# Optimization experiments

Hardware: AMD Instinct MI355X
Metric: run time of the kernel (lower is better)

Reference implementation:

```python
import jax, jax.numpy as jnp
import numpy as np
from jax import lax

T = 32
TAU = 2.0
ALPHA = 2.0
V_TH = 1.0
V_RESET = 0.0
MAX_ACTION = 1.0
HID = 750

# ATan surrogate spike function (spikingjelly surrogate.ATan with alpha=2.0)
@jax.custom_vjp
def atan_spike(x):
    return (x >= 0.0).astype(x.dtype)

def _spike_fwd(x):
    return atan_spike(x), x

def _spike_bwd(x, g):
    # d/dx [1/pi * atan(pi/2 * alpha * x) + 1/2] = (alpha/2) / (1 + (pi/2*alpha*x)^2)
    return (g * (ALPHA / 2.0) / (1.0 + (jnp.pi / 2.0 * ALPHA * x) ** 2),)

atan_spike.defvjp(_spike_fwd, _spike_bwd)


def lif_seq(x_seq):
    """MultiStepLIFNode with decay_input=True, hard reset. x_seq: [T,B,D] -> spikes [T,B,D]."""
    def step(v, x):
        h = v + (x - (v - V_RESET)) / TAU  # neuronal_charge
        s = atan_spike(h - V_TH)           # neuronal_fire
        v_new = h * (1.0 - s) + V_RESET * s  # hard reset
        return v_new, s
    v0 = jnp.zeros_like(x_seq[0])
    _, spikes = lax.scan(step, v0, x_seq)
    return spikes


def seq_linear(x_seq, W, b):
    # x_seq: [T,B,I], W: [O,I], b: [O]
    return jnp.einsum('tbi,oi->tbo', x_seq, W) + b


def nonspiking_out(x_seq):
    # NonSpikingLIFNode.forward receives the whole [T,B,D] seq (override bypasses the step loop):
    # v starts at 0 scalar -> v = 0 + (x - (0 - v_reset))/tau = x/tau (v_reset=0), shape [T,B,D]
    return (x_seq + V_RESET) / TAU - 0.0 + 0.0 if False else x_seq / TAU


def setup_inputs() -> dict:
    key = jax.random.key(0)
    ks = jax.random.split(key, 20)
    B, SD, AD, LD = 2048, 256, 64, 128
    def lin(kw, kb, o, i):
        bound = 1.0 / np.sqrt(i)
        W = jax.random.uniform(kw, (o, i), jnp.float32, -bound, bound)
        b = jax.random.uniform(kb, (o,), jnp.float32, -bound, bound)
        return W, b
    W1, b1 = lin(ks[0], ks[1], HID, SD + AD)
    W2, b2 = lin(ks[2], ks[3], HID, HID)
    Wm, bm = lin(ks[4], ks[5], LD, HID)
    Wls, bls = lin(ks[6], ks[7], LD, HID)
    Wd1, bd1 = lin(ks[8], ks[9], HID, SD + LD)
    Wd2, bd2 = lin(ks[10], ks[11], HID, HID)
    Wd3, bd3 = lin(ks[12], ks[13], AD, HID)
    return {
        'state': jax.random.normal(ks[14], (B, SD), jnp.float32),
        'action': jax.random.normal(ks[15], (B, AD), jnp.float32),
        'eps': jax.random.normal(ks[16], (B, LD), jnp.float32),
        'W1': W1, 'b1': b1, 'W2': W2, 'b2': b2,
        'Wm': Wm, 'bm': bm, 'Wls': Wls, 'bls': bls,
        'Wd1': Wd1, 'bd1': bd1, 'Wd2': Wd2, 'bd2': bd2, 'Wd3': Wd3, 'bd3': bd3,
    }


def reference(state, action, eps, W1, b1, W2, b2, Wm, bm, Wls, bls, Wd1, bd1, Wd2, bd2, Wd3, bd3):
    B = state.shape[0]
    # Encoder
    x = jnp.concatenate([state, action], axis=1)            # [B, SD+AD]
    x_seq = jnp.broadcast_to(x, (T,) + x.shape)             # repeat(T,1,1)
    z = lif_seq(seq_linear(x_seq, W1, b1))                  # e1
    z = lif_seq(seq_linear(z, W2, b2))                      # e2
    mean = jnp.max(seq_linear(z, Wm, bm) / TAU, axis=0)     # NonSpiking v = x/tau, then max over T
    log_std = jnp.max(seq_linear(z, Wls, bls) / TAU, axis=0)
    log_std = jnp.clip(log_std, -4.0, 15.0)
    std = jnp.exp(log_std)
    zlat = mean + std * eps
    # Decoder
    d_in = jnp.concatenate([state, zlat], axis=1)
    d_seq = jnp.broadcast_to(d_in, (T,) + d_in.shape)
    a = lif_seq(seq_linear(d_seq, Wd1, bd1))
    a = lif_seq(seq_linear(a, Wd2, bd2))
    a = jnp.max(seq_linear(a, Wd3, bd3) / TAU, axis=0)
    u = MAX_ACTION * jnp.tanh(a)
    return (u, mean, std)
```

## Files before the change

kernel.cpp:

```cpp
#include <hip/hip_runtime.h>
#include <math.h>

#define TT   32
#define NB   2048
#define SDIM 256
#define ADIM 64
#define LDIM 128
#define HID  750
#define KP   768
#define KW   24
#define EIN  320
#define DIN  384
#define NSTEP 12

typedef float    f32x4 __attribute__((ext_vector_type(4)));
typedef int      i32x4 __attribute__((ext_vector_type(4)));
typedef unsigned u32x4 __attribute__((ext_vector_type(4)));

__device__ __forceinline__ f32x4 mfma16(u32x4 a, u32x4 b, f32x4 c) {
    asm("v_mfma_f32_16x16x32_bf16 %0, %1, %2, %0" : "+v"(c) : "v"(a), "v"(b));
    return c;
}
__device__ __forceinline__ i32x4 mfma_i8(u32x4 a, u32x4 b, i32x4 c) {
    asm("v_mfma_i32_16x16x64_i8 %0, %1, %2, %0" : "+v"(c) : "v"(a), "v"(b));
    return c;
}

__device__ __forceinline__ void gload_lds16(void* lds, const void* g) {
    __builtin_amdgcn_global_load_lds(
        (const __attribute__((address_space(1))) unsigned int*)g,
        (__attribute__((address_space(3))) unsigned int*)lds, 16, 0, 0);
}

__device__ __forceinline__ void bfsplit(float v, unsigned& hb, unsigned& lb) {
    unsigned u = __float_as_uint(v);
    hb = (u + 0x7FFFu + ((u >> 16) & 1u)) >> 16;
    float res = v - __uint_as_float(hb << 16);
    unsigned u2 = __float_as_uint(res);
    lb = (u2 + 0x7FFFu + ((u2 >> 16) & 1u)) >> 16;
}

#define I8_E1 589824
#define I8_E2 1179648
#define I8_E3 1277952
#define I8_E4 1376256
#define I8_E5 1425408
__global__ void wsplit_i8_all(const float* __restrict__ W2,
                              const float* __restrict__ Wd2,
                              const float* __restrict__ Wm,
                              const float* __restrict__ Wls,
                              const float* __restrict__ Wd3,
                              char* __restrict__ W2h,  char* __restrict__ W2l,
                              char* __restrict__ Wd2h, char* __restrict__ Wd2l,
                              char* __restrict__ WmlsH, char* __restrict__ WmlsL,
                              char* __restrict__ Wu3h, char* __restrict__ Wu3l) {
    int i = blockIdx.x * blockDim.x + threadIdx.x;
    if (i >= I8_E5) return;
    const float* src; char* dh; char* dl; int rvalid, o_base;
    if (i < I8_E1)      { src = W2;  dh = W2h;  dl = W2l;  rvalid = HID;  o_base = 0; }
    else if (i < I8_E2) { i -= I8_E1; src = Wd2; dh = Wd2h; dl = Wd2l; rvalid = HID;  o_base = 0; }
    else if (i < I8_E3) { i -= I8_E2; src = Wm;  dh = WmlsH; dl = WmlsL; rvalid = LDIM; o_base = 0; }
    else if (i < I8_E4) { i -= I8_E3; src = Wls; dh = WmlsH; dl = WmlsL; rvalid = LDIM; o_base = 128; }
    else                { i -= I8_E4; src = Wd3; dh = Wu3h; dl = Wu3l; rvalid = ADIM; o_base = 0; }
    int r = i / KP, k = i % KP;
    float v = (r < rvalid && k < HID) ? src[r * HID + k] : 0.f;
    int q = (int)rintf(v * 524288.f);
    int lo = (q << 24) >> 24;
    int hi = (q - lo) >> 8;
    int o = o_base + r;
    size_t di = (size_t)((o >> 6) * NSTEP + (k >> 6)) * 4096
              + ((k >> 4) & 3) * 1024 + (o & 63) * 16 + (k & 15);
    dh[di] = (char)hi;
    dl[di] = (char)lo;
}

#define BF_E1 245760
#define BF_E2 540672
__global__ void wsplit_bf_all(const float* __restrict__ W1,
                              const float* __restrict__ Wd1,
                              unsigned short* __restrict__ W1h,
                              unsigned short* __restrict__ W1l,
                              unsigned short* __restrict__ Wd1h,
                              unsigned short* __restrict__ Wd1l) {
    int i = blockIdx.x * blockDim.x + threadIdx.x;
    if (i >= BF_E2) return;
    const float* src; unsigned short* dh; unsigned short* dl; int K, KS;
    if (i < BF_E1) { src = W1; dh = W1h; dl = W1l; K = EIN; KS = 5; }
    else { i -= BF_E1; src = Wd1; dh = Wd1h; dl = Wd1l; K = DIN; KS = 6; }
    int r = i / K, k = i % K;
    float v = (r < HID) ? src[r * K + k] : 0.f;
    unsigned hb, lb;
    bfsplit(v, hb, lb);
    size_t di = ((size_t)((r >> 6) * KS + (k >> 6)) * 8
               + ((k >> 5) & 1) * 4 + ((k >> 3) & 3)) * 512 + (r & 63) * 8 + (k & 7);
    dh[di] = (unsigned short)hb;
    dl[di] = (unsigned short)lb;
}

__global__ void concat_xsplit_enc(const float* __restrict__ state,
                                  const float* __restrict__ action,
                                  unsigned short* __restrict__ Xh,
                                  unsigned short* __restrict__ Xl) {
    int t = blockIdx.x * blockDim.x + threadIdx.x;
    if (t >= NB * (EIN / 8)) return;
    int b = t & (NB - 1), c8 = t >> 11;
    float vals[8];
    if (c8 < SDIM / 8) {
        const float* src = state + (size_t)b * SDIM + c8 * 8;
#pragma unroll
        for (int j = 0; j < 8; ++j) vals[j] = src[j];
    } else {
        const float* src = action + (size_t)b * ADIM + (c8 * 8 - SDIM);
#pragma unroll
        for (int j = 0; j < 8; ++j) vals[j] = src[j];
    }
    unsigned hs[8], ls[8];
#pragma unroll
    for (int j = 0; j < 8; ++j) bfsplit(vals[j], hs[j], ls[j]);
    u32x4 ph, pl;
#pragma unroll
    for (int j = 0; j < 4; ++j) {
        ph[j] = hs[2 * j] | (hs[2 * j + 1] << 16);
        pl[j] = ls[2 * j] | (ls[2 * j + 1] << 16);
    }
    *(u32x4*)(Xh + (size_t)t * 8) = ph;
    *(u32x4*)(Xl + (size_t)t * 8) = pl;
}

__global__ void latent_xsplit(const float* __restrict__ mean_ws,
                              const float* __restrict__ ls_ws,
                              const float* __restrict__ eps,
                              const float* __restrict__ state,
                              float* __restrict__ out,
                              unsigned short* __restrict__ Xh,
                              unsigned short* __restrict__ Xl) {
    int t = blockIdx.x * blockDim.x + threadIdx.x;
    if (t >= NB * (DIN / 8)) return;
    int b = t & (NB - 1), c8 = t >> 11;
    float vals[8];
    if (c8 < SDIM / 8) {
        const float* src = state + (size_t)b * SDIM + c8 * 8;
#pragma unroll
        for (int j = 0; j < 8; ++j) vals[j] = src[j];
    } else {
        int o0 = c8 * 8 - SDIM;
#pragma unroll
        for (int j = 0; j < 8; ++j) {
            int o = o0 + j;
            float m = mean_ws[(size_t)b * LDIM + o];
            float l = ls_ws[(size_t)b * LDIM + o];
            l = fminf(fmaxf(l, -4.0f), 15.0f);
            float s = expf(l);
            vals[j] = m + s * eps[(size_t)b * LDIM + o];
            out[NB * ADIM + (size_t)b * LDIM + o] = m;
            out[NB * ADIM + NB * LDIM + (size_t)b * LDIM + o] = s;
        }
    }
    unsigned hs[8], ls[8];
#pragma unroll
    for (int j = 0; j < 8; ++j) bfsplit(vals[j], hs[j], ls[j]);
    u32x4 ph, pl;
#pragma unroll
    for (int j = 0; j < 4; ++j) {
        ph[j] = hs[2 * j] | (hs[2 * j + 1] << 16);
        pl[j] = ls[2 * j] | (ls[2 * j + 1] << 16);
    }
    *(u32x4*)(Xh + (size_t)t * 8) = ph;
    *(u32x4*)(Xl + (size_t)t * 8) = pl;
}

template<int KS>
__global__ __launch_bounds__(256)
void lif1(const unsigned short* __restrict__ Ah,
          const unsigned short* __restrict__ Al,
          const unsigned short* __restrict__ Wh,
          const unsigned short* __restrict__ Wl,
          const float* __restrict__ bias,
          unsigned* __restrict__ obitsT) {
    __shared__ __align__(16) char smraw[32768];
    const int tid = threadIdx.x, wave = tid >> 6, l = tid & 63;
    const int kg = l >> 4, li = l & 15;
    const int nb = blockIdx.x, n0 = nb * 64, mb = blockIdx.y;
    const int r0 = mb * 128 + wave * 32;
    f32x4 acc[2][4] = {};

    auto stage = [&](int buf, int step) {
        const char* sH = (const char*)(Wh + (size_t)(nb * KS + step) * 4096);
        const char* sL = (const char*)(Wl + (size_t)(nb * KS + step) * 4096);
        char* d = smraw + buf * 16384;
#pragma unroll
        for (int j = 0; j < 2; ++j) {
            gload_lds16(d + j * 4096 + tid * 16, sH + j * 4096 + tid * 16);
            gload_lds16(d + 8192 + j * 4096 + tid * 16, sL + j * 4096 + tid * 16);
        }
    };

    stage(0, 0);
    for (int step = 0; step < KS; ++step) {
        asm volatile("s_waitcnt vmcnt(0)" ::: "memory");
        __builtin_amdgcn_s_barrier();
        __builtin_amdgcn_sched_barrier(0);
        u32x4 ah[2][2], al2[2][2];
#pragma unroll
        for (int kc = 0; kc < 2; ++kc)
#pragma unroll
            for (int mt = 0; mt < 2; ++mt) {
                int r = r0 + mt * 16 + li;
                size_t aoff = ((size_t)(step * 8 + kc * 4 + kg) * NB + r) * 8;
                ah[kc][mt]  = *(const u32x4*)(Ah + aoff);
                al2[kc][mt] = *(const u32x4*)(Al + aoff);
            }
        if (step + 1 < KS) stage((step + 1) & 1, step + 1);
        const char* bufB = smraw + (step & 1) * 16384;
        __builtin_amdgcn_s_setprio(1);
#pragma unroll
        for (int kc = 0; kc < 2; ++kc) {
#pragma unroll
            for (int nt = 0; nt < 4; ++nt) {
                int boff = (kc * 4 + kg) * 1024 + (nt * 16 + li) * 16;
                u32x4 bh = *(const u32x4*)(bufB + boff);
                u32x4 bl = *(const u32x4*)(bufB + 8192 + boff);
#pragma unroll
                for (int mt = 0; mt < 2; ++mt) {
                    acc[mt][nt] = mfma16(ah[kc][mt], bh, acc[mt][nt]);
                    acc[mt][nt] = mfma16(ah[kc][mt], bl, acc[mt][nt]);
                    acc[mt][nt] = mfma16(al2[kc][mt], bh, acc[mt][nt]);
                }
            }
        }
        __builtin_amdgcn_s_setprio(0);
    }
    __syncthreads();

    unsigned* Sb = (unsigned*)smraw;
#pragma unroll
    for (int nt = 0; nt < 4; ++nt) {
        int o = n0 + nt * 16 + li;
        float bo = (o < HID) ? bias[o] : 0.f;
#pragma unroll
        for (int mt = 0; mt < 2; ++mt)
#pragma unroll
            for (int r = 0; r < 4; ++r) {
                float c = acc[mt][nt][r] + bo;
                float v = 0.f;
                unsigned sb = 0u;
#pragma unroll
                for (int t = 0; t < TT; ++t) {
                    float h = 0.5f * (v + c);
                    if (h >= 1.0f) { sb |= (1u << t); v = 0.f; }
                    else           { v = h; }
                }
                Sb[(wave * 32 + mt * 16 + kg * 4 + r) * 64 + nt * 16 + li] = sb;
            }
    }
    __syncthreads();

    for (int rr = 0; rr < 32; ++rr) {
        int row = wave * 32 + rr;
        unsigned wv = Sb[row * 64 + l];
        unsigned myw = 0;
#pragma unroll
        for (int t = 0; t < TT; ++t) {
            unsigned long long m = __ballot((wv >> t) & 1u);
            if ((l & 31) == t) myw = (l < 32) ? (unsigned)m : (unsigned)(m >> 32);
        }
        int b = mb * 128 + row;
        obitsT[((size_t)b * KW + nb * 2 + (l >= 32)) * TT + (l & 31)] = myw;
    }
}

template<int EPI>
__global__ __launch_bounds__(256)
void bitgemm(const unsigned* __restrict__ bitsT,
             const char* __restrict__ Wh,
             const char* __restrict__ Wl,
             const float* __restrict__ bias,
             const float* __restrict__ bias2,
             unsigned* __restrict__ obitsT,
             float* __restrict__ o0,
             float* __restrict__ o1) {
    __shared__ __align__(16) char smraw[34816];
    const int tid = threadIdx.x;
    const int wave = tid >> 6, l = tid & 63;
    const int kg = l >> 4, li = l & 15;
    const int nb = blockIdx.x, n0 = nb * 64;
    const int by = blockIdx.y;
    const int bb = by * 8 + wave * 2;

    i32x4 acc[4][4][2] = {};

    auto stage = [&](int buf, int step) {
        const char* sH = Wh + (size_t)(nb * NSTEP + step) * 4096;
        const char* sL = Wl + (size_t)(nb * NSTEP + step) * 4096;
        char* d = smraw + buf * 8192;
        gload_lds16(d + tid * 16, sH + tid * 16);
        gload_lds16(d + 4096 + tid * 16, sL + tid * 16);
    };
    auto aidx = [&](int mt, int step) -> size_t {
        int b = bb + (mt >> 1);
        int t = (mt & 1) * 16 + li;
        return ((size_t)b * KW + step * 2 + (kg >> 1)) * TT + t;
    };

    stage(0, 0);
    stage(1, 1);
    unsigned aw[4], awn[4];
#pragma unroll
    for (int mt = 0; mt < 4; ++mt) aw[mt] = bitsT[aidx(mt, 0)];

    for (int step = 0; step < NSTEP; ++step) {
        asm volatile("s_waitcnt vmcnt(6)" ::: "memory");
        __builtin_amdgcn_s_barrier();
        __builtin_amdgcn_sched_barrier(0);
        if (step + 2 < NSTEP) stage((step + 2) % 3, step + 2);
        if (step + 1 < NSTEP) {
#pragma unroll
            for (int mt = 0; mt < 4; ++mt) awn[mt] = bitsT[aidx(mt, step + 1)];
        }
        const char* bufB = smraw + (step % 3) * 8192;
        const unsigned fld = (kg & 1) * 16;
        u32x4 afrag[4];
#pragma unroll
        for (int mt = 0; mt < 4; ++mt) {
            unsigned w = aw[mt] >> fld;
            u32x4 a;
#pragma unroll
            for (int j = 0; j < 4; ++j)
                a[j] = __umul24((w >> (4 * j)) & 0xFu, 0x00204081u) & 0x01010101u;
            afrag[mt] = a;
        }
        __builtin_amdgcn_s_setprio(1);
#pragma unroll
        for (int nt = 0; nt < 4; ++nt) {
            int boff = kg * 1024 + (nt * 16 + li) * 16;
            u32x4 bh = *(const u32x4*)(bufB + boff);
            u32x4 bl = *(const u32x4*)(bufB + 4096 + boff);
#pragma unroll
            for (int mt = 0; mt < 4; ++mt) {
                acc[mt][nt][0] = mfma_i8(afrag[mt], bh, acc[mt][nt][0]);
                acc[mt][nt][1] = mfma_i8(afrag[mt], bl, acc[mt][nt][1]);
            }
        }
        __builtin_amdgcn_s_setprio(0);
#pragma unroll
        for (int mt = 0; mt < 4; ++mt) aw[mt] = awn[mt];
    }
    __syncthreads();

    float* Sf = (float*)smraw;
#pragma unroll
    for (int p = 0; p < 2; ++p) {
#pragma unroll
        for (int mt = 0; mt < 4; ++mt)
#pragma unroll
            for (int ntl = 0; ntl < 2; ++ntl) {
                int nt = p * 2 + ntl;
#pragma unroll
                for (int r = 0; r < 4; ++r) {
                    int cmb = (acc[mt][nt][0][r] << 8) + acc[mt][nt][1][r];
                    Sf[(wave * 64 + mt * 16 + kg * 4 + r) * 34 + ntl * 16 + li]
                        = (float)cmb * (1.f / 524288.f);
                }
            }
        __syncthreads();

        int lb = tid >> 5, col = tid & 31;
        int o = n0 + p * 32 + col;
        int b = by * 8 + lb;
        if (EPI == 0) {
            float bo = (o < HID) ? bias[o] : 0.f;
            float v = 0.f;
            unsigned sb = 0u;
#pragma unroll
            for (int t = 0; t < TT; ++t) {
                float h = 0.5f * (v + Sf[(lb * 32 + t) * 34 + col] + bo);
                if (h >= 1.0f) { sb |= (1u << t); v = 0.f; }
                else           { v = h; }
            }
            if (o >= HID) sb = 0u;
            unsigned myw = 0;
#pragma unroll
            for (int t = 0; t < TT; ++t) {
                unsigned long long m = __ballot((sb >> t) & 1u);
                if ((l & 31) == t) myw = (l < 32) ? (unsigned)m : (unsigned)(m >> 32);
            }
            int bw = by * 8 + wave * 2 + (l >= 32);
            obitsT[((size_t)bw * KW + nb * 2 + p) * TT + (l & 31)] = myw;
        } else {
            float mx = -1e30f;
#pragma unroll
            for (int t = 0; t < TT; ++t)
                mx = fmaxf(mx, Sf[(lb * 32 + t) * 34 + col]);
            if (EPI == 1) {
                float bo = (o < LDIM) ? bias[o] : bias2[o - LDIM];
                float val = 0.5f * (mx + bo);
                if (o < LDIM) o0[(size_t)b * LDIM + o] = val;
                else          o1[(size_t)b * LDIM + (o - LDIM)] = val;
            } else {
                o0[(size_t)b * ADIM + o] = tanhf(0.5f * (mx + bias[o]));
            }
        }
        __syncthreads();
    }
}

extern "C" void kernel_launch(void* const* d_in, const int* in_sizes, int n_in,
                              void* d_out, int out_size, void* d_ws, size_t ws_size,
                              hipStream_t stream) {
    const float* state  = (const float*)d_in[0];
    const float* action = (const float*)d_in[1];
    const float* eps    = (const float*)d_in[2];
    const float* W1  = (const float*)d_in[3];
    const float* b1  = (const float*)d_in[4];
    const float* W2  = (const float*)d_in[5];
    const float* b2  = (const float*)d_in[6];
    const float* Wm  = (const float*)d_in[7];
    const float* bm  = (const float*)d_in[8];
    const float* Wls = (const float*)d_in[9];
    const float* bls = (const float*)d_in[10];
    const float* Wd1 = (const float*)d_in[11];
    const float* bd1 = (const float*)d_in[12];
    const float* Wd2 = (const float*)d_in[13];
    const float* bd2 = (const float*)d_in[14];
    const float* Wd3 = (const float*)d_in[15];
    const float* bd3 = (const float*)d_in[16];
    float* out = (float*)d_out;

    char* ws = (char*)d_ws;
    size_t off = 0;
    auto alloc = [&](size_t bytes) {
        void* p = ws + off;
        off += (bytes + 255) & ~(size_t)255;
        return p;
    };
    unsigned*       bitsT_a = (unsigned*)alloc((size_t)NB * TT * KW * 4);
    unsigned*       bitsT_b = (unsigned*)alloc((size_t)NB * TT * KW * 4);
    float*          mean_ws = (float*)   alloc((size_t)NB * LDIM * 4);
    float*          ls_ws   = (float*)   alloc((size_t)NB * LDIM * 4);
    unsigned short* Xh      = (unsigned short*)alloc((size_t)NB * DIN * 2);
    unsigned short* Xl      = (unsigned short*)alloc((size_t)NB * DIN * 2);
    char*           W2h     = (char*)alloc((size_t)KP * KP);
    char*           W2l     = (char*)alloc((size_t)KP * KP);
    char*           Wd2h    = (char*)alloc((size_t)KP * KP);
    char*           Wd2l    = (char*)alloc((size_t)KP * KP);
    char*           WmlsH   = (char*)alloc((size_t)256 * KP);
    char*           WmlsL   = (char*)alloc((size_t)256 * KP);
    char*           Wu3h    = (char*)alloc((size_t)64 * KP);
    char*           Wu3l    = (char*)alloc((size_t)64 * KP);
    unsigned short* W1h     = (unsigned short*)alloc((size_t)KP * EIN * 2);
    unsigned short* W1l     = (unsigned short*)alloc((size_t)KP * EIN * 2);
    unsigned short* Wd1h    = (unsigned short*)alloc((size_t)KP * DIN * 2);
    unsigned short* Wd1l    = (unsigned short*)alloc((size_t)KP * DIN * 2);

    dim3 blk(256);

    wsplit_i8_all<<<(I8_E5 + 255) / 256, blk, 0, stream>>>(
        W2, Wd2, Wm, Wls, Wd3, W2h, W2l, Wd2h, Wd2l, WmlsH, WmlsL, Wu3h, Wu3l);
    wsplit_bf_all<<<(BF_E2 + 255) / 256, blk, 0, stream>>>(
        W1, Wd1, W1h, W1l, Wd1h, Wd1l);

    concat_xsplit_enc<<<(NB * (EIN / 8) + 255) / 256, blk, 0, stream>>>(state, action, Xh, Xl);
    lif1<5><<<dim3(12, 16), blk, 0, stream>>>(Xh, Xl, W1h, W1l, b1, bitsT_a);
    bitgemm<0><<<dim3(12, NB / 8), blk, 0, stream>>>(bitsT_a, W2h, W2l, b2, nullptr,
                                                     bitsT_b, nullptr, nullptr);
    bitgemm<1><<<dim3(4, NB / 8), blk, 0, stream>>>(bitsT_b, WmlsH, WmlsL, bm, bls,
                                                    nullptr, mean_ws, ls_ws);
    latent_xsplit<<<(NB * (DIN / 8) + 255) / 256, blk, 0, stream>>>(
        mean_ws, ls_ws, eps, state, out, Xh, Xl);

    lif1<6><<<dim3(12, 16), blk, 0, stream>>>(Xh, Xl, Wd1h, Wd1l, bd1, bitsT_a);
    bitgemm<0><<<dim3(12, NB / 8), blk, 0, stream>>>(bitsT_a, Wd2h, Wd2l, bd2, nullptr,
                                                     bitsT_b, nullptr, nullptr);
    bitgemm<2><<<dim3(1, NB / 8), blk, 0, stream>>>(bitsT_b, Wu3h, Wu3l, bd3, nullptr,
                                                    nullptr, out, nullptr);
}
```

Before: 263.5 us.

## Halve bitgemm batch tile to one row per wave with four-deep LDS ring

```diff
diff --git a/kernel.cpp b/kernel.cpp
--- a/kernel.cpp
+++ b/kernel.cpp
@@ -279,54 +279,39 @@
              unsigned* __restrict__ obitsT,
              float* __restrict__ o0,
              float* __restrict__ o1) {
-    __shared__ __align__(16) char smraw[34816];
+    __shared__ __align__(16) char smraw[32768];
     const int tid = threadIdx.x;
-    const int wave = tid >> 6, l = tid & 63;
+    const int w = tid >> 6, l = tid & 63;
     const int kg = l >> 4, li = l & 15;
     const int nb = blockIdx.x, n0 = nb * 64;
     const int by = blockIdx.y;
-    const int bb = by * 8 + wave * 2;
-
-    i32x4 acc[4][4][2] = {};
-
-    auto stage = [&](int buf, int step) {
-        const char* sH = Wh + (size_t)(nb * NSTEP + step) * 4096;
-        const char* sL = Wl + (size_t)(nb * NSTEP + step) * 4096;
-        char* d = smraw + buf * 8192;
+    const int b = by * 4 + w;
+    const unsigned fld = (kg & 1) * 16;
+
+    i32x4 acc[2][4][2] = {};
+
+    auto stage = [&](int s) {
+        char* d = smraw + (s & 3) * 8192;
+        const char* sH = Wh + (size_t)(nb * NSTEP + s) * 4096;
+        const char* sL = Wl + (size_t)(nb * NSTEP + s) * 4096;
         gload_lds16(d + tid * 16, sH + tid * 16);
         gload_lds16(d + 4096 + tid * 16, sL + tid * 16);
     };
-    auto aidx = [&](int mt, int step) -> size_t {
-        int b = bb + (mt >> 1);
-        int t = (mt & 1) * 16 + li;
-        return ((size_t)b * KW + step * 2 + (kg >> 1)) * TT + t;
+    auto loadA = [&](int s, unsigned (&aw)[2]) {
+#pragma unroll
+        for (int mt = 0; mt < 2; ++mt)
+            aw[mt] = bitsT[((size_t)b * KW + s * 2 + (kg >> 1)) * TT + mt * 16 + li];
     };
-
-    stage(0, 0);
-    stage(1, 1);
-    unsigned aw[4], awn[4];
-#pragma unroll
-    for (int mt = 0; mt < 4; ++mt) aw[mt] = bitsT[aidx(mt, 0)];
-
-    for (int step = 0; step < NSTEP; ++step) {
-        asm volatile("s_waitcnt vmcnt(6)" ::: "memory");
-        __builtin_amdgcn_s_barrier();
-        __builtin_amdgcn_sched_barrier(0);
-        if (step + 2 < NSTEP) stage((step + 2) % 3, step + 2);
-        if (step + 1 < NSTEP) {
-#pragma unroll
-            for (int mt = 0; mt < 4; ++mt) awn[mt] = bitsT[aidx(mt, step + 1)];
-        }
-        const char* bufB = smraw + (step % 3) * 8192;
-        const unsigned fld = (kg & 1) * 16;
-        u32x4 afrag[4];
-#pragma unroll
-        for (int mt = 0; mt < 4; ++mt) {
-            unsigned w = aw[mt] >> fld;
+    auto compute = [&](int s, const unsigned (&aw)[2]) {
+        const char* bufB = smraw + (s & 3) * 8192;
+        u32x4 afrag[2];
+#pragma unroll
+        for (int mt = 0; mt < 2; ++mt) {
+            unsigned wv = aw[mt] >> fld;
             u32x4 a;
 #pragma unroll
             for (int j = 0; j < 4; ++j)
-                a[j] = __umul24((w >> (4 * j)) & 0xFu, 0x00204081u) & 0x01010101u;
+                a[j] = __umul24((wv >> (4 * j)) & 0xFu, 0x00204081u) & 0x01010101u;
             afrag[mt] = a;
         }
         __builtin_amdgcn_s_setprio(1);
@@ -336,14 +321,30 @@
             u32x4 bh = *(const u32x4*)(bufB + boff);
             u32x4 bl = *(const u32x4*)(bufB + 4096 + boff);
 #pragma unroll
-            for (int mt = 0; mt < 4; ++mt) {
+            for (int mt = 0; mt < 2; ++mt) {
                 acc[mt][nt][0] = mfma_i8(afrag[mt], bh, acc[mt][nt][0]);
                 acc[mt][nt][1] = mfma_i8(afrag[mt], bl, acc[mt][nt][1]);
             }
         }
         __builtin_amdgcn_s_setprio(0);
-#pragma unroll
-        for (int mt = 0; mt < 4; ++mt) aw[mt] = awn[mt];
+    };
+
+    unsigned aw[2], awn[2];
+    stage(0);
+    asm volatile("s_waitcnt vmcnt(0)" ::: "memory");
+    __builtin_amdgcn_s_barrier();
+    stage(1);
+    loadA(0, aw);
+
+    for (int s = 0; s < NSTEP; ++s) {
+        asm volatile("s_waitcnt vmcnt(4)" ::: "memory");
+        __builtin_amdgcn_s_barrier();
+        __builtin_amdgcn_sched_barrier(0);
+        if (s + 2 < NSTEP) stage(s + 2);
+        if (s + 1 < NSTEP) loadA(s + 1, awn);
+        compute(s, aw);
+        aw[0] = awn[0];
+        aw[1] = awn[1];
     }
     __syncthreads();
 
@@ -351,53 +352,53 @@
 #pragma unroll
     for (int p = 0; p < 2; ++p) {
 #pragma unroll
-        for (int mt = 0; mt < 4; ++mt)
+        for (int mt = 0; mt < 2; ++mt)
 #pragma unroll
             for (int ntl = 0; ntl < 2; ++ntl) {
                 int nt = p * 2 + ntl;
 #pragma unroll
                 for (int r = 0; r < 4; ++r) {
                     int cmb = (acc[mt][nt][0][r] << 8) + acc[mt][nt][1][r];
-                    Sf[(wave * 64 + mt * 16 + kg * 4 + r) * 34 + ntl * 16 + li]
+                    Sf[(w * 32 + mt * 16 + kg * 4 + r) * 34 + ntl * 16 + li]
                         = (float)cmb * (1.f / 524288.f);
                 }
             }
         __syncthreads();
 
-        int lb = tid >> 5, col = tid & 31;
-        int o = n0 + p * 32 + col;
-        int b = by * 8 + lb;
-        if (EPI == 0) {
-            float bo = (o < HID) ? bias[o] : 0.f;
-            float v = 0.f;
-            unsigned sb = 0u;
-#pragma unroll
-            for (int t = 0; t < TT; ++t) {
-                float h = 0.5f * (v + Sf[(lb * 32 + t) * 34 + col] + bo);
-                if (h >= 1.0f) { sb |= (1u << t); v = 0.f; }
-                else           { v = h; }
-            }
-            if (o >= HID) sb = 0u;
-            unsigned myw = 0;
-#pragma unroll
-            for (int t = 0; t < TT; ++t) {
-                unsigned long long m = __ballot((sb >> t) & 1u);
-                if ((l & 31) == t) myw = (l < 32) ? (unsigned)m : (unsigned)(m >> 32);
-            }
-            int bw = by * 8 + wave * 2 + (l >= 32);
-            obitsT[((size_t)bw * KW + nb * 2 + p) * TT + (l & 31)] = myw;
-        } else {
-            float mx = -1e30f;
-#pragma unroll
-            for (int t = 0; t < TT; ++t)
-                mx = fmaxf(mx, Sf[(lb * 32 + t) * 34 + col]);
-            if (EPI == 1) {
-                float bo = (o < LDIM) ? bias[o] : bias2[o - LDIM];
-                float val = 0.5f * (mx + bo);
-                if (o < LDIM) o0[(size_t)b * LDIM + o] = val;
-                else          o1[(size_t)b * LDIM + (o - LDIM)] = val;
+        if (l < 32) {
+            int c = l;
+            int o = n0 + p * 32 + c;
+            if (EPI == 0) {
+                float bo = (o < HID) ? bias[o] : 0.f;
+                float v = 0.f;
+                unsigned sb = 0u;
+#pragma unroll
+                for (int t = 0; t < TT; ++t) {
+                    float h = 0.5f * (v + Sf[(w * 32 + t) * 34 + c] + bo);
+                    if (h >= 1.0f) { sb |= (1u << t); v = 0.f; }
+                    else           { v = h; }
+                }
+                if (o >= HID) sb = 0u;
+                unsigned myw = 0;
+#pragma unroll
+                for (int t = 0; t < TT; ++t) {
+                    unsigned long long m = __ballot((sb >> t) & 1u);
+                    if (l == t) myw = (unsigned)m;
+                }
+                obitsT[((size_t)b * KW + nb * 2 + p) * TT + l] = myw;
             } else {
-                o0[(size_t)b * ADIM + o] = tanhf(0.5f * (mx + bias[o]));
+                float mx = -1e30f;
+#pragma unroll
+                for (int t = 0; t < TT; ++t)
+                    mx = fmaxf(mx, Sf[(w * 32 + t) * 34 + c]);
+                if (EPI == 1) {
+                    float bo = (o < LDIM) ? bias[o] : bias2[o - LDIM];
+                    float val = 0.5f * (mx + bo);
+                    if (o < LDIM) o0[(size_t)b * LDIM + o] = val;
+                    else          o1[(size_t)b * LDIM + (o - LDIM)] = val;
+                } else {
+                    o0[(size_t)b * ADIM + o] = tanhf(0.5f * (mx + bias[o]));
+                }
             }
         }
         __syncthreads();
@@ -461,16 +462,16 @@
 
     concat_xsplit_enc<<<(NB * (EIN / 8) + 255) / 256, blk, 0, stream>>>(state, action, Xh, Xl);
     lif1<5><<<dim3(12, 16), blk, 0, stream>>>(Xh, Xl, W1h, W1l, b1, bitsT_a);
-    bitgemm<0><<<dim3(12, NB / 8), blk, 0, stream>>>(bitsT_a, W2h, W2l, b2, nullptr,
+    bitgemm<0><<<dim3(12, NB / 4), blk, 0, stream>>>(bitsT_a, W2h, W2l, b2, nullptr,
                                                      bitsT_b, nullptr, nullptr);
-    bitgemm<1><<<dim3(4, NB / 8), blk, 0, stream>>>(bitsT_b, WmlsH, WmlsL, bm, bls,
+    bitgemm<1><<<dim3(4, NB / 4), blk, 0, stream>>>(bitsT_b, WmlsH, WmlsL, bm, bls,
                                                     nullptr, mean_ws, ls_ws);
     latent_xsplit<<<(NB * (DIN / 8) + 255) / 256, blk, 0, stream>>>(
         mean_ws, ls_ws, eps, state, out, Xh, Xl);
 
     lif1<6><<<dim3(12, 16), blk, 0, stream>>>(Xh, Xl, Wd1h, Wd1l, bd1, bitsT_a);
-    bitgemm<0><<<dim3(12, NB / 8), blk, 0, stream>>>(bitsT_a, Wd2h, Wd2l, bd2, nullptr,
+    bitgemm<0><<<dim3(12, NB / 4), blk, 0, stream>>>(bitsT_a, Wd2h, Wd2l, bd2, nullptr,
                                                      bitsT_b, nullptr, nullptr);
-    bitgemm<2><<<dim3(1, NB / 8), blk, 0, stream>>>(bitsT_b, Wu3h, Wu3l, bd3, nullptr,
+    bitgemm<2><<<dim3(1, NB / 4), blk, 0, stream>>>(bitsT_b, Wu3h, Wu3l, bd3, nullptr,
                                                     nullptr, out, nullptr);
 }
```

Measured after the change: 269.1 us. +2.1%, slower.
